# Kernel tuning notes

Measured on AMD Instinct MI355X. Metric: run time of the kernel, lower is better.

The kernel has to match this reference:

```python
import jax, jax.numpy as jnp
import numpy as np

EPS = 1e-5
NUM_GROUPS = 8


def setup_inputs() -> dict:
    key = jax.random.key(0)
    ks = jax.random.split(key, 8)
    B, C, H, W = 4, 64, 64, 64
    scale_w = 1.0 / np.sqrt(C)  # roughly xavier scale for [C,C]
    return {
        "x": jax.random.normal(ks[0], (B, C, H, W), dtype=jnp.float32),
        "gamma": jnp.ones((C,), dtype=jnp.float32),
        "beta": jnp.zeros((C,), dtype=jnp.float32),
        "Wq": jax.random.normal(ks[1], (C, C), dtype=jnp.float32) * scale_w,
        "bq": jnp.zeros((C,), dtype=jnp.float32),
        "Wk": jax.random.normal(ks[2], (C, C), dtype=jnp.float32) * scale_w,
        "bk": jnp.zeros((C,), dtype=jnp.float32),
        "Wv": jax.random.normal(ks[3], (C, C), dtype=jnp.float32) * scale_w,
        "bv": jnp.zeros((C,), dtype=jnp.float32),
        "Wp": jax.random.normal(ks[4], (C, C), dtype=jnp.float32) * scale_w,
        "bp": jnp.zeros((C,), dtype=jnp.float32),
    }


def _group_norm(x, gamma, beta):
    # x: [B, C, H, W]; normalize over (C//G, H, W) within each of G groups
    B, C, H, W = x.shape
    xg = x.reshape(B, NUM_GROUPS, -1)
    mean = jnp.mean(xg, axis=-1, keepdims=True)
    var = jnp.var(xg, axis=-1, keepdims=True)
    xn = ((xg - mean) * jax.lax.rsqrt(var + EPS)).reshape(B, C, H, W)
    return xn * gamma[None, :, None, None] + beta[None, :, None, None]


def reference(x, gamma, beta, Wq, bq, Wk, bk, Wv, bv, Wp, bp):
    B, C, H, W = x.shape
    N = H * W
    xn = _group_norm(x, gamma, beta).reshape(B, C, N)  # [B, C, N]
    # 1x1 convs == per-pixel linear maps over channels
    q = jnp.einsum('oc,bcn->bon', Wq, xn) + bq[None, :, None]  # [B, C, N]
    k = jnp.einsum('oc,bcn->bon', Wk, xn) + bk[None, :, None]
    v = jnp.einsum('oc,bcn->bon', Wv, xn) + bv[None, :, None]
    scale = 1.0 / jnp.sqrt(jnp.asarray(C, dtype=x.dtype))
    attn = jnp.einsum('bcn,bcm->bnm', q, k) * scale  # [B, N, N]
    attn = jax.nn.softmax(attn, axis=-1)
    out = jnp.einsum('bnm,bcm->bcn', attn, v)  # [B, C, N]
    out = jnp.einsum('oc,bcn->bon', Wp, out) + bp[None, :, None]
    return x + out.reshape(B, C, H, W)
```

## Files before the change

### kernel.cpp

```cpp
#include <hip/hip_runtime.h>
#include <math.h>

#define B_ 4
#define C_ 64
#define N_ 4096

typedef unsigned short u16;
typedef __attribute__((ext_vector_type(8))) short bf16x8;
typedef __attribute__((ext_vector_type(4))) float f32x4;
typedef __attribute__((ext_vector_type(16))) float f32x16;
typedef __attribute__((ext_vector_type(2))) int i32x2;

__device__ __forceinline__ u16 f2bf(float f) {
    unsigned u = __float_as_uint(f);
    u += 0x7fff + ((u >> 16) & 1);
    return (u16)(u >> 16);
}
__device__ __forceinline__ float bf2f(u16 h) {
    return __uint_as_float(((unsigned)h) << 16);
}

__global__ __launch_bounds__(256) void gn_reduce(const float* __restrict__ x,
                                                 float* __restrict__ partials) {
    int bg = blockIdx.x >> 3, chunk = blockIdx.x & 7;
    const float4* xv = (const float4*)(x + (size_t)bg * 32768 + (size_t)chunk * 4096);
    float s = 0.f, ss = 0.f;
    #pragma unroll
    for (int k = 0; k < 4; k++) {
        float4 v = xv[threadIdx.x + 256 * k];
        s += v.x + v.y + v.z + v.w;
        ss += v.x * v.x + v.y * v.y + v.z * v.z + v.w * v.w;
    }
    #pragma unroll
    for (int off = 1; off < 64; off <<= 1) {
        s += __shfl_xor(s, off);
        ss += __shfl_xor(ss, off);
    }
    __shared__ float red[2][4];
    int w = threadIdx.x >> 6;
    if ((threadIdx.x & 63) == 0) { red[0][w] = s; red[1][w] = ss; }
    __syncthreads();
    if (threadIdx.x == 0) {
        s = red[0][0] + red[0][1] + red[0][2] + red[0][3];
        ss = red[1][0] + red[1][1] + red[1][2] + red[1][3];
        partials[bg * 16 + chunk * 2] = s;
        partials[bg * 16 + chunk * 2 + 1] = ss;
    }
}

__global__ __launch_bounds__(256) void qkv_kernel(
    const float* __restrict__ x, const float* __restrict__ gamma,
    const float* __restrict__ beta, const float* __restrict__ partials,
    const float* __restrict__ Wq, const float* __restrict__ bq,
    const float* __restrict__ Wk, const float* __restrict__ bk,
    const float* __restrict__ Wv, const float* __restrict__ bv,
    u16* __restrict__ Qo, u16* __restrict__ Kf, u16* __restrict__ Vf) {
    __shared__ __align__(16) u16 wt[3][64][64];
    __shared__ __align__(16) u16 xs[64][64];
    __shared__ __align__(16) u16 odt[64][72];

    const int b = (blockIdx.x >> 1) & 3;
    const int nt = ((blockIdx.x >> 3) << 1) | (blockIdx.x & 1);
    const int tid = threadIdx.x;
    const float* Ws[3] = {Wq, Wk, Wv};
    const float* bs[3] = {bq, bk, bv};

    {
        const int rw = tid >> 2, qd = tid & 3;
        #pragma unroll
        for (int s = 0; s < 3; s++) {
            const float4* wsrc = (const float4*)(Ws[s] + rw * 64 + qd * 16);
            float4 f0 = wsrc[0], f1 = wsrc[1], f2 = wsrc[2], f3 = wsrc[3];
            u16 pk[16];
            pk[0]=f2bf(f0.x); pk[1]=f2bf(f0.y); pk[2]=f2bf(f0.z); pk[3]=f2bf(f0.w);
            pk[4]=f2bf(f1.x); pk[5]=f2bf(f1.y); pk[6]=f2bf(f1.z); pk[7]=f2bf(f1.w);
            pk[8]=f2bf(f2.x); pk[9]=f2bf(f2.y); pk[10]=f2bf(f2.z); pk[11]=f2bf(f2.w);
            pk[12]=f2bf(f3.x); pk[13]=f2bf(f3.y); pk[14]=f2bf(f3.z); pk[15]=f2bf(f3.w);
            int blk0 = (2 * qd) ^ (rw & 7), blk1 = (2 * qd + 1) ^ (rw & 7);
            *(uint4*)&wt[s][rw][blk0 * 8] = *(uint4*)&pk[0];
            *(uint4*)&wt[s][rw][blk1 * 8] = *(uint4*)&pk[8];
        }
    }
    {
        const int c = tid >> 2, px0 = (tid & 3) * 16;
        const int g = c >> 3, bg = b * 8 + g;
        float s = 0.f, ss = 0.f;
        #pragma unroll
        for (int i = 0; i < 8; i++) {
            s += partials[bg * 16 + i * 2];
            ss += partials[bg * 16 + i * 2 + 1];
        }
        float mean = s * (1.f / 32768.f);
        float var = ss * (1.f / 32768.f) - mean * mean;
        float rstd = rsqrtf(var + 1e-5f);
        float ga = gamma[c] * rstd;
        float bb = beta[c] - mean * ga;
        const float4* xp = (const float4*)(x + ((size_t)(b * 64 + c)) * N_ + nt * 64 + px0);
        float4 q0 = xp[0], q1 = xp[1], q2 = xp[2], q3 = xp[3];
        float vals[16] = {q0.x,q0.y,q0.z,q0.w, q1.x,q1.y,q1.z,q1.w,
                          q2.x,q2.y,q2.z,q2.w, q3.x,q3.y,q3.z,q3.w};
        #pragma unroll
        for (int e = 0; e < 16; e++) {
            int px = px0 + e;
            xs[px][((c >> 3) ^ (px & 7)) * 8 + (c & 7)] = f2bf(vals[e] * ga + bb);
        }
    }
    __syncthreads();

    const int lane = tid & 63, w = tid >> 6;
    const int lr = lane & 15, lg = lane >> 4;
    const f32x4 zz = {0.f, 0.f, 0.f, 0.f};
    const int sa0 = (lg ^ (lr & 7)) * 8, sa1 = ((4 | lg) ^ (lr & 7)) * 8;

    #pragma unroll
    for (int s = 0; s < 3; s++) {
        bf16x8 a0 = *(const bf16x8*)&wt[s][w * 16 + lr][sa0];
        bf16x8 a1 = *(const bf16x8*)&wt[s][w * 16 + lr][sa1];
        float bias[4];
        #pragma unroll
        for (int r = 0; r < 4; r++) bias[r] = bs[s][w * 16 + lg * 4 + r];
        #pragma unroll
        for (int pt = 0; pt < 4; pt++) {
            bf16x8 b0 = *(const bf16x8*)&xs[pt * 16 + lr][sa0];
            bf16x8 b1 = *(const bf16x8*)&xs[pt * 16 + lr][sa1];
            f32x4 acc = __builtin_amdgcn_mfma_f32_16x16x32_bf16(a0, b0, zz, 0, 0, 0);
            acc = __builtin_amdgcn_mfma_f32_16x16x32_bf16(a1, b1, acc, 0, 0, 0);
            if (s == 0) {
                #pragma unroll
                for (int r = 0; r < 4; r++)
                    odt[pt * 16 + lr][w * 16 + lg * 4 + r] = f2bf((acc[r] + bias[r]) * 0.18033688f);
            } else if (s == 1) {
                #pragma unroll
                for (int r = 0; r < 4; r++)
                    odt[pt * 16 + lr][w * 16 + lg * 4 + r] = f2bf(acc[r] + bias[r]);
            } else {
                #pragma unroll
                for (int r = 0; r < 4; r++)
                    odt[w * 16 + lg * 4 + r][pt * 16 + lr] = f2bf(acc[r] + bias[r]);
            }
        }
        __syncthreads();
        if (s == 0) {
            u16* dst = Qo + ((size_t)(b * N_ + nt * 64)) * 64;
            #pragma unroll
            for (int k2 = 0; k2 < 2; k2++) {
                int c = tid + k2 * 256;
                int px = c >> 3, blk = c & 7;
                *(uint4*)(dst + (size_t)px * 64 + blk * 8) = *(const uint4*)&odt[px][blk * 8];
            }
        } else if (s == 1) {
            u16* dst = Kf + ((size_t)(b * 64 + nt)) * 4096;
            #pragma unroll
            for (int k2 = 0; k2 < 2; k2++) {
                int f = tid + k2 * 256;
                int khf = f >> 8, sf = (f >> 6) & 3, lhf = (f >> 5) & 1, l31f = f & 31;
                *(uint4*)(dst + (size_t)f * 8) =
                    *(const uint4*)&odt[khf * 32 + l31f][(sf * 2 + lhf) * 8];
            }
        } else {
            u16* dst = Vf + ((size_t)(b * 64 + nt)) * 4096;
            #pragma unroll
            for (int k2 = 0; k2 < 2; k2++) {
                int f = tid + k2 * 256;
                int khf = f >> 8, cf = (f >> 7) & 1, s2f = (f >> 6) & 1;
                int lhf = (f >> 5) & 1, l31f = f & 31;
                *(uint4*)(dst + (size_t)f * 8) =
                    *(const uint4*)&odt[cf * 32 + l31f][(khf * 4 + s2f * 2 + lhf) * 8];
            }
        }
        __syncthreads();
    }
}

__global__ __launch_bounds__(256, 4) void flash_kernel(
    const u16* __restrict__ Qg, const u16* __restrict__ Kf,
    const u16* __restrict__ Vf, u16* __restrict__ Opart, float* __restrict__ ml,
    int nsplit) {
    __shared__ __align__(16) u16 smem[14336];

    const int b = (blockIdx.x >> 1) & 3;
    const int j = ((blockIdx.x >> 3) << 1) | (blockIdx.x & 1);
    const int sp = j >> 6;
    const int qt = j & 63;
    const int tid = threadIdx.x;
    const int w = tid >> 6, lane = tid & 63;
    const int l31 = lane & 31, lh = lane >> 5;
    const int qh = w >> 1, kh = w & 1;

    const int per = (nsplit == 4) ? 16 : (nsplit == 3) ? 22 : 32;
    const int kt0 = sp * per;
    const int NT = min(per, 64 - kt0);

    const u16* qptr = Qg + ((size_t)(b * N_ + qt * 64 + qh * 32 + l31)) * 64 + lh * 8;
    bf16x8 q0 = *(const bf16x8*)(qptr);
    bf16x8 q1 = *(const bf16x8*)(qptr + 16);
    bf16x8 q2 = *(const bf16x8*)(qptr + 32);
    bf16x8 q3 = *(const bf16x8*)(qptr + 48);

    const u16* kp = Kf + ((size_t)(b * 64 + kt0)) * 4096 + kh * 2048 + lane * 8;
    const u16* vp = Vf + ((size_t)(b * 64 + kt0)) * 4096 + kh * 2048 + lane * 8;

    bf16x8 kf0 = *(const bf16x8*)(kp);
    bf16x8 kf1 = *(const bf16x8*)(kp + 512);
    bf16x8 kf2 = *(const bf16x8*)(kp + 1024);
    bf16x8 kf3 = *(const bf16x8*)(kp + 1536);

    f32x16 o0, o1;
    #pragma unroll
    for (int r = 0; r < 16; r++) { o0[r] = 0.f; o1[r] = 0.f; }
    float lsum = 0.f;

    for (int t = 0; t < NT; ++t) {
        const u16* vtp = vp + (size_t)t * 4096;
        bf16x8 vf0 = *(const bf16x8*)(vtp);
        bf16x8 vf1 = *(const bf16x8*)(vtp + 512);
        bf16x8 vf2 = *(const bf16x8*)(vtp + 1024);
        bf16x8 vf3 = *(const bf16x8*)(vtp + 1536);

        f32x16 st;
        #pragma unroll
        for (int r = 0; r < 16; r++) st[r] = 0.f;
        __builtin_amdgcn_s_setprio(1);
        st = __builtin_amdgcn_mfma_f32_32x32x16_bf16(kf0, q0, st, 0, 0, 0);
        st = __builtin_amdgcn_mfma_f32_32x32x16_bf16(kf1, q1, st, 0, 0, 0);
        st = __builtin_amdgcn_mfma_f32_32x32x16_bf16(kf2, q2, st, 0, 0, 0);
        st = __builtin_amdgcn_mfma_f32_32x32x16_bf16(kf3, q3, st, 0, 0, 0);
        __builtin_amdgcn_s_setprio(0);

        const u16* knp = kp + (size_t)(t + 1) * 4096;
        kf0 = *(const bf16x8*)(knp);
        kf1 = *(const bf16x8*)(knp + 512);
        kf2 = *(const bf16x8*)(knp + 1024);
        kf3 = *(const bf16x8*)(knp + 1536);

        #pragma unroll
        for (int r = 0; r < 16; r++) st[r] = exp2f(st[r] - 12.f);
        lsum += (((st[0]+st[1])+(st[2]+st[3])) + ((st[4]+st[5])+(st[6]+st[7])))
              + (((st[8]+st[9])+(st[10]+st[11])) + ((st[12]+st[13])+(st[14]+st[15])));
        unsigned c0,c1,c2,c3,c4,c5,c6,c7;
        asm("v_cvt_pk_bf16_f32 %0, %1, %2" : "=v"(c0) : "v"(st[0]),  "v"(st[1]));
        asm("v_cvt_pk_bf16_f32 %0, %1, %2" : "=v"(c1) : "v"(st[2]),  "v"(st[3]));
        asm("v_cvt_pk_bf16_f32 %0, %1, %2" : "=v"(c2) : "v"(st[4]),  "v"(st[5]));
        asm("v_cvt_pk_bf16_f32 %0, %1, %2" : "=v"(c3) : "v"(st[6]),  "v"(st[7]));
        asm("v_cvt_pk_bf16_f32 %0, %1, %2" : "=v"(c4) : "v"(st[8]),  "v"(st[9]));
        asm("v_cvt_pk_bf16_f32 %0, %1, %2" : "=v"(c5) : "v"(st[10]), "v"(st[11]));
        asm("v_cvt_pk_bf16_f32 %0, %1, %2" : "=v"(c6) : "v"(st[12]), "v"(st[13]));
        asm("v_cvt_pk_bf16_f32 %0, %1, %2" : "=v"(c7) : "v"(st[14]), "v"(st[15]));
        i32x2 r02 = __builtin_amdgcn_permlane32_swap((int)c0, (int)c2, false, false);
        i32x2 r13 = __builtin_amdgcn_permlane32_swap((int)c1, (int)c3, false, false);
        i32x2 r46 = __builtin_amdgcn_permlane32_swap((int)c4, (int)c6, false, false);
        i32x2 r57 = __builtin_amdgcn_permlane32_swap((int)c5, (int)c7, false, false);
        union U { int u[4]; bf16x8 v; };
        U pa0 = {{r02[0], r13[0], r02[1], r13[1]}};
        U pa1 = {{r46[0], r57[0], r46[1], r57[1]}};

        __builtin_amdgcn_s_setprio(1);
        o0 = __builtin_amdgcn_mfma_f32_32x32x16_bf16(pa0.v, vf0, o0, 0, 0, 0);
        o0 = __builtin_amdgcn_mfma_f32_32x32x16_bf16(pa1.v, vf1, o0, 0, 0, 0);
        o1 = __builtin_amdgcn_mfma_f32_32x32x16_bf16(pa0.v, vf2, o1, 0, 0, 0);
        o1 = __builtin_amdgcn_mfma_f32_32x32x16_bf16(pa1.v, vf3, o1, 0, 0, 0);
        __builtin_amdgcn_s_setprio(0);
    }

    float* red = (float*)smem;
    u16* ost = smem + 10240;
    if (kh == 1) {
        float* dst = red + (qh * 64 + lane) * 34;
        #pragma unroll
        for (int r = 0; r < 16; r++) { dst[r] = o0[r]; dst[16 + r] = o1[r]; }
        dst[32] = lsum;
    }
    __syncthreads();
    if (kh == 0) {
        const float* src = red + (qh * 64 + lane) * 34;
        float l2 = lsum + src[32];
        i32x2 rr = __builtin_amdgcn_permlane32_swap(__float_as_int(l2), __float_as_int(l2), false, false);
        float lpart = __int_as_float(lh ? rr[0] : rr[1]);
        float lfull = l2 + lpart;
        #pragma unroll
        for (int r = 0; r < 16; r++) {
            float v0 = o0[r] + src[r];
            float v1 = o1[r] + src[16 + r];
            int ql = qh * 32 + (r & 3) + 8 * (r >> 2) + 4 * lh;
            ost[ql * 64 + l31] = f2bf(v0);
            ost[ql * 64 + 32 + l31] = f2bf(v1);
        }
        if (lane < 32)
            ml[(size_t)sp * 16384 + b * N_ + qt * 64 + qh * 32 + l31] = lfull;
    }
    __syncthreads();
    uint4* op = (uint4*)(Opart + (size_t)sp * 1048576 + ((size_t)(b * N_ + qt * 64)) * 64);
    const uint4* os4 = (const uint4*)ost;
    op[tid] = os4[tid];
    op[tid + 256] = os4[tid + 256];
}

__global__ __launch_bounds__(256) void proj_kernel(
    const u16* __restrict__ Opart, const float* __restrict__ ml,
    const float* __restrict__ Wp, const float* __restrict__ bp,
    const float* __restrict__ x, float* __restrict__ out, int nsplit) {
    __shared__ __align__(16) u16 wp[64][64];
    __shared__ __align__(16) u16 og[64][64];
    const int b = (blockIdx.x >> 1) & 3;
    const int nt = ((blockIdx.x >> 3) << 1) | (blockIdx.x & 1);
    const int tid = threadIdx.x;

    {
        const int rw = tid >> 2, qd = tid & 3;
        const float4* wsrc = (const float4*)(Wp + rw * 64 + qd * 16);
        float4 f0 = wsrc[0], f1 = wsrc[1], f2 = wsrc[2], f3 = wsrc[3];
        u16 pk[16];
        pk[0]=f2bf(f0.x); pk[1]=f2bf(f0.y); pk[2]=f2bf(f0.z); pk[3]=f2bf(f0.w);
        pk[4]=f2bf(f1.x); pk[5]=f2bf(f1.y); pk[6]=f2bf(f1.z); pk[7]=f2bf(f1.w);
        pk[8]=f2bf(f2.x); pk[9]=f2bf(f2.y); pk[10]=f2bf(f2.z); pk[11]=f2bf(f2.w);
        pk[12]=f2bf(f3.x); pk[13]=f2bf(f3.y); pk[14]=f2bf(f3.z); pk[15]=f2bf(f3.w);
        int blk0 = (2 * qd) ^ (rw & 7), blk1 = (2 * qd + 1) ^ (rw & 7);
        *(uint4*)&wp[rw][blk0 * 8] = *(uint4*)&pk[0];
        *(uint4*)&wp[rw][blk1 * 8] = *(uint4*)&pk[8];
    }
    {
        #pragma unroll
        for (int k2 = 0; k2 < 2; k2++) {
            int cidx = tid + k2 * 256;
            int px = cidx >> 3, blk = cidx & 7;
            int gpix = b * N_ + nt * 64 + px;
            float lsum = 0.f;
            for (int s = 0; s < nsplit; s++) lsum += ml[(size_t)s * 16384 + gpix];
            float inv = 1.f / lsum;
            float acc8[8] = {0.f,0.f,0.f,0.f,0.f,0.f,0.f,0.f};
            for (int s = 0; s < nsplit; s++) {
                u16 ov[8];
                *(uint4*)ov = *(const uint4*)(Opart + (size_t)s * 1048576 + (size_t)gpix * 64 + blk * 8);
                #pragma unroll
                for (int j = 0; j < 8; j++) acc8[j] += bf2f(ov[j]);
            }
            u16 y[8];
            #pragma unroll
            for (int j = 0; j < 8; j++) y[j] = f2bf(acc8[j] * inv);
            *(uint4*)&og[px][(blk ^ (px & 7)) * 8] = *(uint4*)y;
        }
    }
    __syncthreads();

    const int lane = tid & 63, w = tid >> 6;
    const int lr = lane & 15, lg = lane >> 4;
    const f32x4 zz = {0.f, 0.f, 0.f, 0.f};
    const int sa0 = (lg ^ (lr & 7)) * 8, sa1 = ((4 | lg) ^ (lr & 7)) * 8;

    bf16x8 a0 = *(const bf16x8*)&wp[w * 16 + lr][sa0];
    bf16x8 a1 = *(const bf16x8*)&wp[w * 16 + lr][sa1];
    float bias[4];
    #pragma unroll
    for (int r = 0; r < 4; r++) bias[r] = bp[w * 16 + lg * 4 + r];

    #pragma unroll
    for (int pt = 0; pt < 4; pt++) {
        bf16x8 b0 = *(const bf16x8*)&og[pt * 16 + lr][sa0];
        bf16x8 b1 = *(const bf16x8*)&og[pt * 16 + lr][sa1];
        f32x4 acc = __builtin_amdgcn_mfma_f32_16x16x32_bf16(a0, b0, zz, 0, 0, 0);
        acc = __builtin_amdgcn_mfma_f32_16x16x32_bf16(a1, b1, acc, 0, 0, 0);
        #pragma unroll
        for (int r = 0; r < 4; r++) {
            int cout = w * 16 + lg * 4 + r;
            int px = pt * 16 + lr;
            size_t idx = ((size_t)(b * 64 + cout)) * N_ + nt * 64 + px;
            out[idx] = x[idx] + bias[r] + acc[r];
        }
    }
}

extern "C" void kernel_launch(void* const* d_in, const int* in_sizes, int n_in,
                              void* d_out, int out_size, void* d_ws, size_t ws_size,
                              hipStream_t stream) {
    const float* x     = (const float*)d_in[0];
    const float* gamma = (const float*)d_in[1];
    const float* beta  = (const float*)d_in[2];
    const float* Wq    = (const float*)d_in[3];
    const float* bq    = (const float*)d_in[4];
    const float* Wk    = (const float*)d_in[5];
    const float* bk    = (const float*)d_in[6];
    const float* Wv    = (const float*)d_in[7];
    const float* bv    = (const float*)d_in[8];
    const float* Wp    = (const float*)d_in[9];
    const float* bp    = (const float*)d_in[10];
    float* out = (float*)d_out;

    const size_t elems = (size_t)B_ * N_ * C_;
    const size_t base = 4096 + 262144;
    float* partials = (float*)d_ws;
    float* ml = (float*)((char*)d_ws + 4096);
    u16* Qb = (u16*)((char*)d_ws + base);
    u16* Kb = Qb + elems;
    u16* Vt = Kb + elems;
    u16* Opart = Vt + elems;

    const size_t need4 = base + 3 * elems * 2 + 4 * elems * 2;
    const size_t need3 = base + 3 * elems * 2 + 3 * elems * 2;
    const int nsplit = (ws_size >= need4) ? 4 : (ws_size >= need3) ? 3 : 2;

    gn_reduce<<<256, 256, 0, stream>>>(x, partials);
    qkv_kernel<<<256, 256, 0, stream>>>(x, gamma, beta, partials,
                                        Wq, bq, Wk, bk, Wv, bv, Qb, Kb, Vt);
    flash_kernel<<<nsplit * 256, 256, 0, stream>>>(Qb, Kb, Vt, Opart, ml, nsplit);
    proj_kernel<<<256, 256, 0, stream>>>(Opart, ml, Wp, bp, x, out, nsplit);
}
```

Before: 49.72 us.

## Process two query subtiles per wave in flash kernel to reuse K/V fragments

Each flash block now covers 128 queries instead of 64, so every wave computes two 32-query score tiles that share the same K and V register fragments. This halves K/V global loads per query and halves the grid size. V loads are also moved to the end of the iteration as a prefetch for the next tile. The cost is more registers and LDS, so occupancy drops (launch bound lowered to 2) and fewer blocks are available to fill the GPU.

```diff
diff --git a/kernel.cpp b/kernel.cpp
--- a/kernel.cpp
+++ b/kernel.cpp
@@ -18,6 +18,31 @@
 }
 __device__ __forceinline__ float bf2f(u16 h) {
     return __uint_as_float(((unsigned)h) << 16);
+}
+
+__device__ __forceinline__ float softmax_pack(f32x16& st, bf16x8& p0, bf16x8& p1) {
+    #pragma unroll
+    for (int r = 0; r < 16; r++) st[r] = exp2f(st[r] - 12.f);
+    float s = (((st[0]+st[1])+(st[2]+st[3])) + ((st[4]+st[5])+(st[6]+st[7])))
+            + (((st[8]+st[9])+(st[10]+st[11])) + ((st[12]+st[13])+(st[14]+st[15])));
+    unsigned c0,c1,c2,c3,c4,c5,c6,c7;
+    asm("v_cvt_pk_bf16_f32 %0, %1, %2" : "=v"(c0) : "v"(st[0]),  "v"(st[1]));
+    asm("v_cvt_pk_bf16_f32 %0, %1, %2" : "=v"(c1) : "v"(st[2]),  "v"(st[3]));
+    asm("v_cvt_pk_bf16_f32 %0, %1, %2" : "=v"(c2) : "v"(st[4]),  "v"(st[5]));
+    asm("v_cvt_pk_bf16_f32 %0, %1, %2" : "=v"(c3) : "v"(st[6]),  "v"(st[7]));
+    asm("v_cvt_pk_bf16_f32 %0, %1, %2" : "=v"(c4) : "v"(st[8]),  "v"(st[9]));
+    asm("v_cvt_pk_bf16_f32 %0, %1, %2" : "=v"(c5) : "v"(st[10]), "v"(st[11]));
+    asm("v_cvt_pk_bf16_f32 %0, %1, %2" : "=v"(c6) : "v"(st[12]), "v"(st[13]));
+    asm("v_cvt_pk_bf16_f32 %0, %1, %2" : "=v"(c7) : "v"(st[14]), "v"(st[15]));
+    i32x2 r02 = __builtin_amdgcn_permlane32_swap((int)c0, (int)c2, false, false);
+    i32x2 r13 = __builtin_amdgcn_permlane32_swap((int)c1, (int)c3, false, false);
+    i32x2 r46 = __builtin_amdgcn_permlane32_swap((int)c4, (int)c6, false, false);
+    i32x2 r57 = __builtin_amdgcn_permlane32_swap((int)c5, (int)c7, false, false);
+    union U { int u[4]; bf16x8 v; };
+    U a = {{r02[0], r13[0], r02[1], r13[1]}};
+    U b2 = {{r46[0], r57[0], r46[1], r57[1]}};
+    p0 = a.v; p1 = b2.v;
+    return s;
 }
 
 __global__ __launch_bounds__(256) void gn_reduce(const float* __restrict__ x,
@@ -172,16 +197,16 @@
     }
 }
 
-__global__ __launch_bounds__(256, 4) void flash_kernel(
+__global__ __launch_bounds__(256, 2) void flash_kernel(
     const u16* __restrict__ Qg, const u16* __restrict__ Kf,
     const u16* __restrict__ Vf, u16* __restrict__ Opart, float* __restrict__ ml,
     int nsplit) {
-    __shared__ __align__(16) u16 smem[14336];
+    __shared__ __align__(16) u16 smem[25088];
 
     const int b = (blockIdx.x >> 1) & 3;
     const int j = ((blockIdx.x >> 3) << 1) | (blockIdx.x & 1);
-    const int sp = j >> 6;
-    const int qt = j & 63;
+    const int sp = j >> 5;
+    const int qt2 = j & 31;
     const int tid = threadIdx.x;
     const int w = tid >> 6, lane = tid & 63;
     const int l31 = lane & 31, lh = lane >> 5;
@@ -191,11 +216,16 @@
     const int kt0 = sp * per;
     const int NT = min(per, 64 - kt0);
 
-    const u16* qptr = Qg + ((size_t)(b * N_ + qt * 64 + qh * 32 + l31)) * 64 + lh * 8;
-    bf16x8 q0 = *(const bf16x8*)(qptr);
-    bf16x8 q1 = *(const bf16x8*)(qptr + 16);
-    bf16x8 q2 = *(const bf16x8*)(qptr + 32);
-    bf16x8 q3 = *(const bf16x8*)(qptr + 48);
+    const u16* qptrA = Qg + ((size_t)(b * N_ + qt2 * 128 + qh * 64 + l31)) * 64 + lh * 8;
+    const u16* qptrB = qptrA + 32 * 64;
+    bf16x8 qa0 = *(const bf16x8*)(qptrA);
+    bf16x8 qa1 = *(const bf16x8*)(qptrA + 16);
+    bf16x8 qa2 = *(const bf16x8*)(qptrA + 32);
+    bf16x8 qa3 = *(const bf16x8*)(qptrA + 48);
+    bf16x8 qb0 = *(const bf16x8*)(qptrB);
+    bf16x8 qb1 = *(const bf16x8*)(qptrB + 16);
+    bf16x8 qb2 = *(const bf16x8*)(qptrB + 32);
+    bf16x8 qb3 = *(const bf16x8*)(qptrB + 48);
 
     const u16* kp = Kf + ((size_t)(b * 64 + kt0)) * 4096 + kh * 2048 + lane * 8;
     const u16* vp = Vf + ((size_t)(b * 64 + kt0)) * 4096 + kh * 2048 + lane * 8;
@@ -204,27 +234,29 @@
     bf16x8 kf1 = *(const bf16x8*)(kp + 512);
     bf16x8 kf2 = *(const bf16x8*)(kp + 1024);
     bf16x8 kf3 = *(const bf16x8*)(kp + 1536);
-
-    f32x16 o0, o1;
-    #pragma unroll
-    for (int r = 0; r < 16; r++) { o0[r] = 0.f; o1[r] = 0.f; }
-    float lsum = 0.f;
+    bf16x8 vf0 = *(const bf16x8*)(vp);
+    bf16x8 vf1 = *(const bf16x8*)(vp + 512);
+    bf16x8 vf2 = *(const bf16x8*)(vp + 1024);
+    bf16x8 vf3 = *(const bf16x8*)(vp + 1536);
+
+    f32x16 oa0, oa1, ob0, ob1;
+    #pragma unroll
+    for (int r = 0; r < 16; r++) { oa0[r] = 0.f; oa1[r] = 0.f; ob0[r] = 0.f; ob1[r] = 0.f; }
+    float lsa = 0.f, lsb = 0.f;
 
     for (int t = 0; t < NT; ++t) {
-        const u16* vtp = vp + (size_t)t * 4096;
-        bf16x8 vf0 = *(const bf16x8*)(vtp);
-        bf16x8 vf1 = *(const bf16x8*)(vtp + 512);
-        bf16x8 vf2 = *(const bf16x8*)(vtp + 1024);
-        bf16x8 vf3 = *(const bf16x8*)(vtp + 1536);
-
-        f32x16 st;
-        #pragma unroll
-        for (int r = 0; r < 16; r++) st[r] = 0.f;
+        f32x16 sta, stb;
+        #pragma unroll
+        for (int r = 0; r < 16; r++) { sta[r] = 0.f; stb[r] = 0.f; }
         __builtin_amdgcn_s_setprio(1);
-        st = __builtin_amdgcn_mfma_f32_32x32x16_bf16(kf0, q0, st, 0, 0, 0);
-        st = __builtin_amdgcn_mfma_f32_32x32x16_bf16(kf1, q1, st, 0, 0, 0);
-        st = __builtin_amdgcn_mfma_f32_32x32x16_bf16(kf2, q2, st, 0, 0, 0);
-        st = __builtin_amdgcn_mfma_f32_32x32x16_bf16(kf3, q3, st, 0, 0, 0);
+        sta = __builtin_amdgcn_mfma_f32_32x32x16_bf16(kf0, qa0, sta, 0, 0, 0);
+        sta = __builtin_amdgcn_mfma_f32_32x32x16_bf16(kf1, qa1, sta, 0, 0, 0);
+        sta = __builtin_amdgcn_mfma_f32_32x32x16_bf16(kf2, qa2, sta, 0, 0, 0);
+        sta = __builtin_amdgcn_mfma_f32_32x32x16_bf16(kf3, qa3, sta, 0, 0, 0);
+        stb = __builtin_amdgcn_mfma_f32_32x32x16_bf16(kf0, qb0, stb, 0, 0, 0);
+        stb = __builtin_amdgcn_mfma_f32_32x32x16_bf16(kf1, qb1, stb, 0, 0, 0);
+        stb = __builtin_amdgcn_mfma_f32_32x32x16_bf16(kf2, qb2, stb, 0, 0, 0);
+        stb = __builtin_amdgcn_mfma_f32_32x32x16_bf16(kf3, qb3, stb, 0, 0, 0);
         __builtin_amdgcn_s_setprio(0);
 
         const u16* knp = kp + (size_t)(t + 1) * 4096;
@@ -233,66 +265,75 @@
         kf2 = *(const bf16x8*)(knp + 1024);
         kf3 = *(const bf16x8*)(knp + 1536);
 
-        #pragma unroll
-        for (int r = 0; r < 16; r++) st[r] = exp2f(st[r] - 12.f);
-        lsum += (((st[0]+st[1])+(st[2]+st[3])) + ((st[4]+st[5])+(st[6]+st[7])))
-              + (((st[8]+st[9])+(st[10]+st[11])) + ((st[12]+st[13])+(st[14]+st[15])));
-        unsigned c0,c1,c2,c3,c4,c5,c6,c7;
-        asm("v_cvt_pk_bf16_f32 %0, %1, %2" : "=v"(c0) : "v"(st[0]),  "v"(st[1]));
-        asm("v_cvt_pk_bf16_f32 %0, %1, %2" : "=v"(c1) : "v"(st[2]),  "v"(st[3]));
-        asm("v_cvt_pk_bf16_f32 %0, %1, %2" : "=v"(c2) : "v"(st[4]),  "v"(st[5]));
-        asm("v_cvt_pk_bf16_f32 %0, %1, %2" : "=v"(c3) : "v"(st[6]),  "v"(st[7]));
-        asm("v_cvt_pk_bf16_f32 %0, %1, %2" : "=v"(c4) : "v"(st[8]),  "v"(st[9]));
-        asm("v_cvt_pk_bf16_f32 %0, %1, %2" : "=v"(c5) : "v"(st[10]), "v"(st[11]));
-        asm("v_cvt_pk_bf16_f32 %0, %1, %2" : "=v"(c6) : "v"(st[12]), "v"(st[13]));
-        asm("v_cvt_pk_bf16_f32 %0, %1, %2" : "=v"(c7) : "v"(st[14]), "v"(st[15]));
-        i32x2 r02 = __builtin_amdgcn_permlane32_swap((int)c0, (int)c2, false, false);
-        i32x2 r13 = __builtin_amdgcn_permlane32_swap((int)c1, (int)c3, false, false);
-        i32x2 r46 = __builtin_amdgcn_permlane32_swap((int)c4, (int)c6, false, false);
-        i32x2 r57 = __builtin_amdgcn_permlane32_swap((int)c5, (int)c7, false, false);
-        union U { int u[4]; bf16x8 v; };
-        U pa0 = {{r02[0], r13[0], r02[1], r13[1]}};
-        U pa1 = {{r46[0], r57[0], r46[1], r57[1]}};
-
+        bf16x8 paa0, paa1;
+        lsa += softmax_pack(sta, paa0, paa1);
         __builtin_amdgcn_s_setprio(1);
-        o0 = __builtin_amdgcn_mfma_f32_32x32x16_bf16(pa0.v, vf0, o0, 0, 0, 0);
-        o0 = __builtin_amdgcn_mfma_f32_32x32x16_bf16(pa1.v, vf1, o0, 0, 0, 0);
-        o1 = __builtin_amdgcn_mfma_f32_32x32x16_bf16(pa0.v, vf2, o1, 0, 0, 0);
-        o1 = __builtin_amdgcn_mfma_f32_32x32x16_bf16(pa1.v, vf3, o1, 0, 0, 0);
+        oa0 = __builtin_amdgcn_mfma_f32_32x32x16_bf16(paa0, vf0, oa0, 0, 0, 0);
+        oa0 = __builtin_amdgcn_mfma_f32_32x32x16_bf16(paa1, vf1, oa0, 0, 0, 0);
+        oa1 = __builtin_amdgcn_mfma_f32_32x32x16_bf16(paa0, vf2, oa1, 0, 0, 0);
+        oa1 = __builtin_amdgcn_mfma_f32_32x32x16_bf16(paa1, vf3, oa1, 0, 0, 0);
         __builtin_amdgcn_s_setprio(0);
+
+        bf16x8 pab0, pab1;
+        lsb += softmax_pack(stb, pab0, pab1);
+        __builtin_amdgcn_s_setprio(1);
+        ob0 = __builtin_amdgcn_mfma_f32_32x32x16_bf16(pab0, vf0, ob0, 0, 0, 0);
+        ob0 = __builtin_amdgcn_mfma_f32_32x32x16_bf16(pab1, vf1, ob0, 0, 0, 0);
+        ob1 = __builtin_amdgcn_mfma_f32_32x32x16_bf16(pab0, vf2, ob1, 0, 0, 0);
+        ob1 = __builtin_amdgcn_mfma_f32_32x32x16_bf16(pab1, vf3, ob1, 0, 0, 0);
+        __builtin_amdgcn_s_setprio(0);
+
+        const u16* vnp = vp + (size_t)(t + 1) * 4096;
+        vf0 = *(const bf16x8*)(vnp);
+        vf1 = *(const bf16x8*)(vnp + 512);
+        vf2 = *(const bf16x8*)(vnp + 1024);
+        vf3 = *(const bf16x8*)(vnp + 1536);
     }
 
     float* red = (float*)smem;
-    u16* ost = smem + 10240;
+    u16* ost = smem + 16896;
     if (kh == 1) {
-        float* dst = red + (qh * 64 + lane) * 34;
-        #pragma unroll
-        for (int r = 0; r < 16; r++) { dst[r] = o0[r]; dst[16 + r] = o1[r]; }
-        dst[32] = lsum;
+        float* dst = red + (qh * 64 + lane) * 66;
+        #pragma unroll
+        for (int r = 0; r < 16; r++) {
+            dst[r] = oa0[r]; dst[16 + r] = oa1[r];
+            dst[32 + r] = ob0[r]; dst[48 + r] = ob1[r];
+        }
+        dst[64] = lsa; dst[65] = lsb;
     }
     __syncthreads();
     if (kh == 0) {
-        const float* src = red + (qh * 64 + lane) * 34;
-        float l2 = lsum + src[32];
-        i32x2 rr = __builtin_amdgcn_permlane32_swap(__float_as_int(l2), __float_as_int(l2), false, false);
-        float lpart = __int_as_float(lh ? rr[0] : rr[1]);
-        float lfull = l2 + lpart;
+        const float* src = red + (qh * 64 + lane) * 66;
+        float la = lsa + src[64];
+        float lb = lsb + src[65];
+        i32x2 ra = __builtin_amdgcn_permlane32_swap(__float_as_int(la), __float_as_int(la), false, false);
+        float lfa = la + __int_as_float(lh ? ra[0] : ra[1]);
+        i32x2 rb = __builtin_amdgcn_permlane32_swap(__float_as_int(lb), __float_as_int(lb), false, false);
+        float lfb = lb + __int_as_float(lh ? rb[0] : rb[1]);
         #pragma unroll
         for (int r = 0; r < 16; r++) {
-            float v0 = o0[r] + src[r];
-            float v1 = o1[r] + src[16 + r];
-            int ql = qh * 32 + (r & 3) + 8 * (r >> 2) + 4 * lh;
-            ost[ql * 64 + l31] = f2bf(v0);
-            ost[ql * 64 + 32 + l31] = f2bf(v1);
-        }
-        if (lane < 32)
-            ml[(size_t)sp * 16384 + b * N_ + qt * 64 + qh * 32 + l31] = lfull;
+            float va0 = oa0[r] + src[r];
+            float va1 = oa1[r] + src[16 + r];
+            float vb0 = ob0[r] + src[32 + r];
+            float vb1 = ob1[r] + src[48 + r];
+            int qra = qh * 64 + (r & 3) + 8 * (r >> 2) + 4 * lh;
+            int qrb = qra + 32;
+            ost[qra * 64 + l31] = f2bf(va0);
+            ost[qra * 64 + 32 + l31] = f2bf(va1);
+            ost[qrb * 64 + l31] = f2bf(vb0);
+            ost[qrb * 64 + 32 + l31] = f2bf(vb1);
+        }
+        if (lane < 32) {
+            float* mlp = ml + (size_t)sp * 16384 + b * N_ + qt2 * 128 + qh * 64;
+            mlp[l31] = lfa;
+            mlp[32 + l31] = lfb;
+        }
     }
     __syncthreads();
-    uint4* op = (uint4*)(Opart + (size_t)sp * 1048576 + ((size_t)(b * N_ + qt * 64)) * 64);
+    uint4* op = (uint4*)(Opart + (size_t)sp * 1048576 + ((size_t)(b * N_ + qt2 * 128)) * 64);
     const uint4* os4 = (const uint4*)ost;
-    op[tid] = os4[tid];
-    op[tid + 256] = os4[tid + 256];
+    #pragma unroll
+    for (int k = 0; k < 4; k++) op[tid + k * 256] = os4[tid + k * 256];
 }
 
 __global__ __launch_bounds__(256) void proj_kernel(
@@ -401,6 +442,6 @@
     gn_reduce<<<256, 256, 0, stream>>>(x, partials);
     qkv_kernel<<<256, 256, 0, stream>>>(x, gamma, beta, partials,
                                         Wq, bq, Wk, bk, Wv, bv, Qb, Kb, Vt);
-    flash_kernel<<<nsplit * 256, 256, 0, stream>>>(Qb, Kb, Vt, Opart, ml, nsplit);
+    flash_kernel<<<nsplit * 128, 256, 0, stream>>>(Qb, Kb, Vt, Opart, ml, nsplit);
     proj_kernel<<<256, 256, 0, stream>>>(Opart, ml, Wp, bp, x, out, nsplit);
 }
```

New measurement: 54.08 us. +8.8%, slower.
